# Performance work log

Measured on AMD Instinct MI355X. Metric: run time of the kernel, lower is better.

Reference implementation:

```python
import jax, jax.numpy as jnp
import numpy as np

B = 128
H = 512
S_TOK = 512
S_DESC = 128
N_NODES = 65536
MARGIN = 0.05
COS_EPS = 1e-8


def setup_inputs() -> dict:
    key = jax.random.key(0)
    ks = jax.random.split(key, 26)
    sc = 1.0 / np.sqrt(H)
    inp = {
        "token_feat": jax.random.normal(ks[0], (B, S_TOK, H), jnp.float32),
        "token_len": jnp.maximum(jax.random.randint(ks[1], (B,), 0, S_TOK), 1),
        "node_h": jax.random.normal(ks[2], (N_NODES, H), jnp.float32),
        "seg_ids": jnp.sort(jax.random.randint(ks[3], (N_NODES,), 0, B)),
        "desc_anchor_feat": jax.random.normal(ks[4], (B, S_DESC, H), jnp.float32),
        "desc_anchor_len": jnp.maximum(jax.random.randint(ks[5], (B,), 0, S_DESC), 1),
        "desc_neg_feat": jax.random.normal(ks[6], (B, S_DESC, H), jnp.float32),
        "desc_neg_len": jnp.maximum(jax.random.randint(ks[7], (B,), 0, S_DESC), 1),
        # attention params: Linear(H,H) weight/bias, Linear(H,1) weight/bias
        "Wt": jax.random.normal(ks[8], (H, H), jnp.float32) * sc,
        "bt": jax.random.normal(ks[9], (H,), jnp.float32) * sc,
        "vt": jax.random.normal(ks[10], (H,), jnp.float32) * sc,
        "ct": jax.random.normal(ks[11], (), jnp.float32) * sc,
        "Wa": jax.random.normal(ks[12], (H, H), jnp.float32) * sc,
        "ba": jax.random.normal(ks[13], (H,), jnp.float32) * sc,
        "va": jax.random.normal(ks[14], (H,), jnp.float32) * sc,
        "ca": jax.random.normal(ks[15], (), jnp.float32) * sc,
        "Wd": jax.random.normal(ks[16], (H, H), jnp.float32) * sc,
        "bd": jax.random.normal(ks[17], (H,), jnp.float32) * sc,
        "vd": jax.random.normal(ks[18], (H,), jnp.float32) * sc,
        "cd": jax.random.normal(ks[19], (), jnp.float32) * sc,
        "Wf": jax.random.normal(ks[20], (2 * H, H), jnp.float32) * sc,
        "bf": jax.random.normal(ks[21], (H,), jnp.float32) * sc,
    }
    return inp


def masked_attn_pool(feat, lens, W, b, v, c):
    # feat: [B,S,H]; lens: [B]. Masked softmax attention pooling == the
    # per-sample masked_select + softmax + bmm loop, vectorized.
    logits = jnp.einsum("bsh,h->bs", jnp.tanh(jnp.einsum("bsh,hk->bsk", feat, W) + b), v) + c
    mask = jnp.arange(feat.shape[1])[None, :] < lens[:, None]
    logits = jnp.where(mask, logits, -jnp.inf)
    w = jax.nn.softmax(logits, axis=1)  # [B,S]
    return jnp.einsum("bs,bsh->bh", w, feat)


def segment_attn_pool(h, seg, W, b, v, c, num_segments):
    # h: [N,H] packed node states; seg: [N] sample id. Per-segment softmax attn
    # pooling == the per-sample slice + softmax + bmm loop over tree_node_num.
    logits = jnp.tanh(h @ W + b) @ v + c  # [N]
    m = jax.ops.segment_max(logits, seg, num_segments=num_segments)
    e = jnp.exp(logits - m[seg])
    denom = jax.ops.segment_sum(e, seg, num_segments=num_segments)
    w = e / denom[seg]
    return jax.ops.segment_sum(w[:, None] * h, seg, num_segments=num_segments)


def cosine_sim(a, b):
    na = jnp.maximum(jnp.linalg.norm(a, axis=1), COS_EPS)
    nb = jnp.maximum(jnp.linalg.norm(b, axis=1), COS_EPS)
    return jnp.sum(a * b, axis=1) / (na * nb)


def reference(token_feat, token_len, node_h, seg_ids, desc_anchor_feat,
              desc_anchor_len, desc_neg_feat, desc_neg_len,
              Wt, bt, vt, ct, Wa, ba, va, ca, Wd, bd, vd, cd, Wf, bf):
    # token modality (use_token_attn, then use_tanh)
    tok = jnp.tanh(masked_attn_pool(token_feat, token_len, Wt, bt, vt, ct))
    # AST modality: use_tanh applies to node states BEFORE attention
    hn = jnp.tanh(node_h)
    ast = jnp.tanh(segment_attn_pool(hn, seg_ids, Wa, ba, va, ca, B))
    code_feat = jnp.tanh(jnp.concatenate([tok, ast], axis=1) @ Wf + bf)
    # desc modality: attn pool, use_tanh, then the extra unconditional tanh
    da = jnp.tanh(jnp.tanh(masked_attn_pool(desc_anchor_feat, desc_anchor_len, Wd, bd, vd, cd)))
    dn = jnp.tanh(jnp.tanh(masked_attn_pool(desc_neg_feat, desc_neg_len, Wd, bd, vd, cd)))
    anchor_sim = cosine_sim(code_feat, da)
    neg_sim = cosine_sim(code_feat, dn)
    loss = jnp.mean(jnp.maximum(MARGIN - anchor_sim + neg_sim, 1e-6))
    return loss
```

## Files before the change

kernel.cpp:

```cpp
#include <hip/hip_runtime.h>
#include <math.h>

#define HDIM 512
#define BATCH 128

typedef _Float16 f16x8 __attribute__((ext_vector_type(8)));
typedef float f32x4 __attribute__((ext_vector_type(4)));

__device__ __forceinline__ float fast_tanh(float x) {
  float e = __expf(2.0f * x);
  return 1.0f - 2.0f / (e + 1.0f);
}

__device__ __forceinline__ void gload_lds16(const void* g, void* l) {
  __builtin_amdgcn_global_load_lds(
      (const __attribute__((address_space(1))) unsigned int*)g,
      (__attribute__((address_space(3))) unsigned int*)l, 16, 0, 0);
}

__global__ __launch_bounds__(256) void cvt_w3_kernel(
    const float* __restrict__ Wt, const float* __restrict__ Wa,
    const float* __restrict__ Wd, _Float16* __restrict__ W2t,
    _Float16* __restrict__ W2a, _Float16* __restrict__ W2d) {
  const int i = blockIdx.x * 256 + threadIdx.x;
  if (i >= 512 * 64) return;
  const float* W = (blockIdx.y == 0) ? Wt : (blockIdx.y == 1) ? Wa : Wd;
  _Float16* W2 = (blockIdx.y == 0) ? W2t : (blockIdx.y == 1) ? W2a : W2d;
  const int n = i & 511, g = i >> 9;
  const int kt = g >> 2, kc = g & 3;
  f16x8 h;
#pragma unroll
  for (int j = 0; j < 8; ++j)
    h[j] = (_Float16)W[(size_t)(kt * 32 + kc * 8 + j) * HDIM + n];
  char* dst = (char*)W2 + (size_t)kt * 32768 + n * 64 + ((kc * 16) ^ ((n & 3) << 4));
  *(f16x8*)dst = h;
}

__global__ __launch_bounds__(512, 1) void gemm_logits_merged_kernel(
    const float* __restrict__ A_tok, const float* __restrict__ A_node,
    const float* __restrict__ A_da, const float* __restrict__ A_dn,
    const _Float16* __restrict__ W2t, const _Float16* __restrict__ W2a,
    const _Float16* __restrict__ W2d,
    const float* __restrict__ bt, const float* __restrict__ vt,
    const float* __restrict__ ba, const float* __restrict__ va,
    const float* __restrict__ bd, const float* __restrict__ vd,
    float* __restrict__ logits_tok, float* __restrict__ logits_node,
    float* __restrict__ logits_desc) {
  __shared__ __align__(16) _Float16 As[2][128 * 32];
  __shared__ __align__(16) _Float16 Bs[2][512 * 32];

  const int tid = threadIdx.x;
  const int raw = (int)blockIdx.x;
  const int swz = (raw & 7) * 160 + (raw >> 3);

  int id, mb;
  if (swz < 512)       { id = 0; mb = swz; }
  else if (swz < 1024) { id = 1; mb = swz - 512; }
  else if (swz < 1152) { id = 2; mb = swz - 1024; }
  else                 { id = 3; mb = swz - 1152; }
  const float* A = (id == 0) ? A_tok : (id == 1) ? A_node : (id == 2) ? A_da : A_dn;
  const _Float16* W2 = (id == 0) ? W2t : (id == 1) ? W2a : W2d;
  const float* bias = (id == 0) ? bt : (id == 1) ? ba : bd;
  const float* vvec = (id == 0) ? vt : (id == 1) ? va : vd;
  float* logits = (id == 0) ? logits_tok
                : (id == 1) ? logits_node
                : (id == 2) ? logits_desc : (logits_desc + 16384);
  const bool do_tanh = (id == 1);
  const size_t m0 = (size_t)mb * 128;

  const int lane = tid & 63, wid = tid >> 6;
  const int tx = lane & 15, qd = lane >> 4;

  const int arow = tid >> 2;
  const int apart = tid & 3;
  const float* arowp = A + (m0 + arow) * HDIM + apart * 8;
  const int awbyte = arow * 64 + ((apart * 16) ^ ((arow & 3) << 4));

  f32x4 acc[8][4];
#pragma unroll
  for (int i = 0; i < 8; ++i)
#pragma unroll
    for (int j = 0; j < 4; ++j) acc[i][j] = (f32x4){0.f, 0.f, 0.f, 0.f};

  float4 ar0, ar1;
  auto LOAD_A = [&](int t) {
    const float* p = arowp + t * 32;
    ar0 = ((const float4*)p)[0];
    ar1 = ((const float4*)p)[1];
  };
  auto STAGE_B = [&](int buf, int t) {
    const char* b = (const char*)W2 + (size_t)t * 32768;
#pragma unroll
    for (int p = 0; p < 4; ++p)
      gload_lds16(b + tid * 16 + p * 8192, (char*)Bs[buf] + tid * 16 + p * 8192);
  };
  auto WRITE_A = [&](int buf) {
    float v0 = ar0.x, v1 = ar0.y, v2 = ar0.z, v3 = ar0.w;
    float v4 = ar1.x, v5 = ar1.y, v6 = ar1.z, v7 = ar1.w;
    if (do_tanh) {
      v0 = fast_tanh(v0); v1 = fast_tanh(v1); v2 = fast_tanh(v2); v3 = fast_tanh(v3);
      v4 = fast_tanh(v4); v5 = fast_tanh(v5); v6 = fast_tanh(v6); v7 = fast_tanh(v7);
    }
    f16x8 h;
    h[0] = (_Float16)v0; h[1] = (_Float16)v1; h[2] = (_Float16)v2; h[3] = (_Float16)v3;
    h[4] = (_Float16)v4; h[5] = (_Float16)v5; h[6] = (_Float16)v6; h[7] = (_Float16)v7;
    *(f16x8*)((char*)As[buf] + awbyte) = h;
  };
  auto COMPUTE = [&](int buf) {
    f16x8 aF[8], bF[4];
#pragma unroll
    for (int i = 0; i < 8; ++i) {
      const int row = i * 16 + tx;
      aF[i] = *(const f16x8*)((const char*)As[buf] + row * 64 + ((qd * 16) ^ ((row & 3) << 4)));
    }
#pragma unroll
    for (int j = 0; j < 4; ++j) {
      const int n = wid * 64 + j * 16 + tx;
      bF[j] = *(const f16x8*)((const char*)Bs[buf] + n * 64 + ((qd * 16) ^ ((n & 3) << 4)));
    }
    __builtin_amdgcn_s_setprio(1);
#pragma unroll
    for (int i = 0; i < 8; ++i)
#pragma unroll
      for (int j = 0; j < 4; ++j)
        acc[i][j] = __builtin_amdgcn_mfma_f32_16x16x32_f16(aF[i], bF[j], acc[i][j], 0, 0, 0);
    __builtin_amdgcn_s_setprio(0);
  };

  LOAD_A(0);
  STAGE_B(0, 0);
  WRITE_A(0);
  __syncthreads();

  for (int t = 0; t < 16; ++t) {
    const int cur = t & 1;
    if (t < 15) {
      LOAD_A(t + 1);
      STAGE_B(cur ^ 1, t + 1);
    }
    COMPUTE(cur);
    if (t < 15) WRITE_A(cur ^ 1);
    __syncthreads();
  }

  float vv[4], bb[4];
#pragma unroll
  for (int j = 0; j < 4; ++j) {
    const int n = wid * 64 + j * 16 + tx;
    vv[j] = vvec[n];
    bb[j] = bias[n];
  }
  float* red = (float*)As;
#pragma unroll
  for (int i = 0; i < 8; ++i) {
#pragma unroll
    for (int r = 0; r < 4; ++r) {
      float s = 0.0f;
#pragma unroll
      for (int j = 0; j < 4; ++j)
        s = fmaf(vv[j], fast_tanh(acc[i][j][r] + bb[j]), s);
      s += __shfl_xor(s, 1);
      s += __shfl_xor(s, 2);
      s += __shfl_xor(s, 4);
      s += __shfl_xor(s, 8);
      if (tx == 0) red[wid * 128 + i * 16 + qd * 4 + r] = s;
    }
  }
  __syncthreads();
  if (tid < 128) {
    float tot = 0.0f;
#pragma unroll
    for (int w = 0; w < 8; ++w) tot += red[w * 128 + tid];
    logits[m0 + tid] = tot;
  }
}


__global__ void zero_kernel(float* __restrict__ p, int n) {
  const int i = blockIdx.x * 256 + threadIdx.x;
  if (i < n) p[i] = 0.0f;
}

__global__ void seg_bounds_kernel(const int* __restrict__ seg, int N,
                                  int* __restrict__ seg_start) {
  const int b = threadIdx.x;
  if (b > BATCH) return;
  int lo = 0, hi = N;
  while (lo < hi) {
    const int mid = (lo + hi) >> 1;
    if (seg[mid] < b) lo = mid + 1; else hi = mid;
  }
  seg_start[b] = lo;
}

__global__ __launch_bounds__(256) void softmax_all_kernel(
    float* __restrict__ ltok, float* __restrict__ ldesc,
    float* __restrict__ lnode, const int* __restrict__ tlen,
    const int* __restrict__ dalen, const int* __restrict__ dnlen,
    const int* __restrict__ seg_start) {
  __shared__ float smax[4], ssum[4];
  const int b = blockIdx.x, mode = blockIdx.y, tid = threadIdx.x;
  float* l;
  int s0, s1, fill_end;
  if (mode == 0)      { l = ltok + (size_t)b * 512;          s0 = 0; s1 = tlen[b];  fill_end = 512; }
  else if (mode == 1) { l = ldesc + (size_t)b * 128;         s0 = 0; s1 = dalen[b]; fill_end = 128; }
  else if (mode == 2) { l = ldesc + 16384 + (size_t)b * 128; s0 = 0; s1 = dnlen[b]; fill_end = 128; }
  else                { l = lnode; s0 = seg_start[b]; s1 = seg_start[b + 1]; fill_end = -1; }

  float mymax = -1e30f;
  for (int s = s0 + tid; s < s1; s += 256) mymax = fmaxf(mymax, l[s]);
#pragma unroll
  for (int off = 32; off; off >>= 1) mymax = fmaxf(mymax, __shfl_xor(mymax, off));
  if ((tid & 63) == 0) smax[tid >> 6] = mymax;
  __syncthreads();
  const float bmax = fmaxf(fmaxf(smax[0], smax[1]), fmaxf(smax[2], smax[3]));
  float mysum = 0.0f;
  for (int s = s0 + tid; s < s1; s += 256) mysum += __expf(l[s] - bmax);
#pragma unroll
  for (int off = 32; off; off >>= 1) mysum += __shfl_xor(mysum, off);
  if ((tid & 63) == 0) ssum[tid >> 6] = mysum;
  __syncthreads();
  const float inv = 1.0f / (ssum[0] + ssum[1] + ssum[2] + ssum[3]);
  for (int s = s0 + tid; s < s1; s += 256) l[s] = __expf(l[s] - bmax) * inv;
  if (fill_end > 0)
    for (int s = s1 + tid; s < fill_end; s += 256) l[s] = 0.0f;
}

__global__ __launch_bounds__(256) void pool_masked_all_kernel(
    const float* __restrict__ tok_feat, const float* __restrict__ da_feat,
    const float* __restrict__ dn_feat, const float* __restrict__ ltok,
    const float* __restrict__ ldesc, float* __restrict__ tok_pool,
    float* __restrict__ da_pool, float* __restrict__ dn_pool) {
  const int b = blockIdx.x, c = blockIdx.y, tid = threadIdx.x;
  const float* feat;
  const float* w;
  float* out;
  int S, s0;
  if (c < 8)       { feat = tok_feat; S = 512; w = ltok + (size_t)b * 512;          out = tok_pool; s0 = c * 64; }
  else if (c < 10) { feat = da_feat;  S = 128; w = ldesc + (size_t)b * 128;         out = da_pool;  s0 = (c - 8) * 64; }
  else             { feat = dn_feat;  S = 128; w = ldesc + 16384 + (size_t)b * 128; out = dn_pool;  s0 = (c - 10) * 64; }
  const int h = tid * 2;
  const float* fb = feat + (size_t)b * S * HDIM + h;
  float ax = 0.0f, ay = 0.0f;
  for (int s = s0; s < s0 + 64; ++s) {
    const float wsc = w[s];
    if (wsc != 0.0f) {
      const float2 f = *(const float2*)(fb + (size_t)s * HDIM);
      ax = fmaf(wsc, f.x, ax);
      ay = fmaf(wsc, f.y, ay);
    }
  }
  atomicAdd(&out[b * HDIM + h], ax);
  atomicAdd(&out[b * HDIM + h + 1], ay);
}

__global__ __launch_bounds__(256) void pool_seg_kernel(
    const float* __restrict__ node_h, const float* __restrict__ w,
    const int* __restrict__ seg_start, float* __restrict__ pool) {
  const int b = blockIdx.x, c = blockIdx.y, tid = threadIdx.x;
  const int h = tid * 2;
  const int s0 = seg_start[b], s1 = seg_start[b + 1];
  const int nseg = s1 - s0;
  const int chunk = (nseg + (int)gridDim.y - 1) / (int)gridDim.y;
  const int a0 = s0 + c * chunk;
  const int a1 = min(s1, a0 + chunk);
  float ax = 0.0f, ay = 0.0f;
  for (int s = a0; s < a1; ++s) {
    const float wsc = w[s];
    const float2 f = *(const float2*)(node_h + (size_t)s * HDIM + h);
    ax = fmaf(wsc, fast_tanh(f.x), ax);
    ay = fmaf(wsc, fast_tanh(f.y), ay);
  }
  atomicAdd(&pool[b * HDIM + h], ax);
  atomicAdd(&pool[b * HDIM + h + 1], ay);
}

__global__ __launch_bounds__(256) void code_gemm_kernel(
    const float* __restrict__ tok_pool, const float* __restrict__ ast_pool,
    const float* __restrict__ Wf, float* __restrict__ parts) {
  __shared__ float catS[128][65];
  __shared__ float4 wfS[64][32];
  const int nb = blockIdx.x, kb = blockIdx.y, tid = threadIdx.x;
  const int k0 = kb * 64;
  const float* src = (k0 < 512) ? (tok_pool + k0) : (ast_pool + (k0 - 512));
  for (int i = tid; i < 128 * 16; i += 256) {
    const int r = i >> 4, c4 = i & 15;
    const float4 v = *(const float4*)(src + (size_t)r * HDIM + c4 * 4);
    catS[r][c4 * 4 + 0] = fast_tanh(v.x);
    catS[r][c4 * 4 + 1] = fast_tanh(v.y);
    catS[r][c4 * 4 + 2] = fast_tanh(v.z);
    catS[r][c4 * 4 + 3] = fast_tanh(v.w);
  }
  for (int i = tid; i < 64 * 32; i += 256) {
    const int r = i >> 5, c = i & 31;
    wfS[r][c] = *(const float4*)(Wf + (size_t)(k0 + r) * HDIM + nb * 128 + c * 4);
  }
  __syncthreads();
  const int tb = tid >> 4, tn = tid & 15;
  const int b0 = tb * 8, n0l = tn * 8;
  float acc[8][8];
#pragma unroll
  for (int i = 0; i < 8; ++i)
#pragma unroll
    for (int j = 0; j < 8; ++j) acc[i][j] = 0.0f;
  for (int k = 0; k < 64; ++k) {
    float a[8];
#pragma unroll
    for (int i = 0; i < 8; ++i) a[i] = catS[b0 + i][k];
    const float4 w0 = wfS[k][tn * 2], w1 = wfS[k][tn * 2 + 1];
    const float wv[8] = {w0.x, w0.y, w0.z, w0.w, w1.x, w1.y, w1.z, w1.w};
#pragma unroll
    for (int i = 0; i < 8; ++i)
#pragma unroll
      for (int j = 0; j < 8; ++j) acc[i][j] = fmaf(a[i], wv[j], acc[i][j]);
  }
  float* dst = parts + ((size_t)kb * 128) * HDIM + nb * 128;
#pragma unroll
  for (int i = 0; i < 8; ++i) {
    const float4 o0 = {acc[i][0], acc[i][1], acc[i][2], acc[i][3]};
    const float4 o1 = {acc[i][4], acc[i][5], acc[i][6], acc[i][7]};
    *(float4*)(dst + (size_t)(b0 + i) * HDIM + n0l) = o0;
    *(float4*)(dst + (size_t)(b0 + i) * HDIM + n0l + 4) = o1;
  }
}

__global__ __launch_bounds__(256) void sims_kernel(
    const float* __restrict__ parts, const float* __restrict__ bfv,
    const float* __restrict__ da_pool, const float* __restrict__ dn_pool,
    float* __restrict__ terms) {
  __shared__ float sr[4][5];
  const int b = blockIdx.x, tid = threadIdx.x;
  float c2 = 0, a2 = 0, n2 = 0, ca = 0, cn = 0;
  for (int i = tid; i < HDIM; i += 256) {
    float pre = bfv[i];
#pragma unroll
    for (int kb = 0; kb < 16; ++kb)
      pre += parts[((size_t)kb * 128 + b) * HDIM + i];
    const float cf = fast_tanh(pre);
    const float av = fast_tanh(fast_tanh(da_pool[(size_t)b * HDIM + i]));
    const float nv = fast_tanh(fast_tanh(dn_pool[(size_t)b * HDIM + i]));
    c2 = fmaf(cf, cf, c2); a2 = fmaf(av, av, a2); n2 = fmaf(nv, nv, n2);
    ca = fmaf(cf, av, ca); cn = fmaf(cf, nv, cn);
  }
#pragma unroll
  for (int off = 32; off; off >>= 1) {
    c2 += __shfl_xor(c2, off); a2 += __shfl_xor(a2, off); n2 += __shfl_xor(n2, off);
    ca += __shfl_xor(ca, off); cn += __shfl_xor(cn, off);
  }
  const int wv = tid >> 6;
  if ((tid & 63) == 0) {
    sr[wv][0] = c2; sr[wv][1] = a2; sr[wv][2] = n2; sr[wv][3] = ca; sr[wv][4] = cn;
  }
  __syncthreads();
  if (tid == 0) {
    c2 = sr[0][0] + sr[1][0] + sr[2][0] + sr[3][0];
    a2 = sr[0][1] + sr[1][1] + sr[2][1] + sr[3][1];
    n2 = sr[0][2] + sr[1][2] + sr[2][2] + sr[3][2];
    ca = sr[0][3] + sr[1][3] + sr[2][3] + sr[3][3];
    cn = sr[0][4] + sr[1][4] + sr[2][4] + sr[3][4];
    const float nc = fmaxf(sqrtf(c2), 1e-8f);
    const float na = fmaxf(sqrtf(a2), 1e-8f);
    const float nn = fmaxf(sqrtf(n2), 1e-8f);
    terms[b] = fmaxf(0.05f - ca / (nc * na) + cn / (nc * nn), 1e-6f);
  }
}

__global__ void loss_kernel(const float* __restrict__ terms, float* __restrict__ out) {
  const int tid = threadIdx.x;
  float v = terms[tid];
#pragma unroll
  for (int off = 32; off; off >>= 1) v += __shfl_xor(v, off);
  __shared__ float sr[2];
  if ((tid & 63) == 0) sr[tid >> 6] = v;
  __syncthreads();
  if (tid == 0) out[0] = (sr[0] + sr[1]) * (1.0f / (float)BATCH);
}


extern "C" void kernel_launch(void* const* d_in, const int* in_sizes, int n_in,
                              void* d_out, int out_size, void* d_ws, size_t ws_size,
                              hipStream_t stream) {
  (void)in_sizes; (void)n_in; (void)out_size; (void)ws_size;
  const float* token_feat = (const float*)d_in[0];
  const int*   token_len  = (const int*)d_in[1];
  const float* node_h     = (const float*)d_in[2];
  const int*   seg_ids    = (const int*)d_in[3];
  const float* da_feat    = (const float*)d_in[4];
  const int*   da_len     = (const int*)d_in[5];
  const float* dn_feat    = (const float*)d_in[6];
  const int*   dn_len     = (const int*)d_in[7];
  const float* Wt = (const float*)d_in[8];
  const float* bt = (const float*)d_in[9];
  const float* vt = (const float*)d_in[10];
  const float* Wa = (const float*)d_in[12];
  const float* ba = (const float*)d_in[13];
  const float* va = (const float*)d_in[14];
  const float* Wd = (const float*)d_in[16];
  const float* bd = (const float*)d_in[17];
  const float* vd = (const float*)d_in[18];
  const float* Wf  = (const float*)d_in[20];
  const float* bfv = (const float*)d_in[21];

  const int MTOK = 65536;
  const int MDESC2 = 32768;
  const int NNODES = 65536;

  float* ws = (float*)d_ws;
  float* logits_tok  = ws;
  float* logits_node = logits_tok + MTOK;
  float* logits_desc = logits_node + NNODES;
  float* tok_pool    = logits_desc + MDESC2;
  float* ast_pool    = tok_pool + 128 * HDIM;
  float* da_pool     = ast_pool + 128 * HDIM;
  float* dn_pool     = da_pool + 128 * HDIM;
  float* terms       = dn_pool + 128 * HDIM;
  int*   seg_start   = (int*)(terms + 128);
  float* parts       = (float*)(seg_start + 256);
  _Float16* W2t = (_Float16*)(parts + 16 * 128 * HDIM);
  _Float16* W2a = W2t + HDIM * HDIM;
  _Float16* W2d = W2a + HDIM * HDIM;

  zero_kernel<<<dim3((4 * 128 * HDIM + 255) / 256), 256, 0, stream>>>(tok_pool, 4 * 128 * HDIM);
  seg_bounds_kernel<<<1, 256, 0, stream>>>(seg_ids, NNODES, seg_start);
  cvt_w3_kernel<<<dim3(128, 3), 256, 0, stream>>>(Wt, Wa, Wd, W2t, W2a, W2d);

  gemm_logits_merged_kernel<<<1280, 512, 0, stream>>>(
      token_feat, node_h, da_feat, dn_feat, W2t, W2a, W2d,
      bt, vt, ba, va, bd, vd, logits_tok, logits_node, logits_desc);

  softmax_all_kernel<<<dim3(BATCH, 4), 256, 0, stream>>>(
      logits_tok, logits_desc, logits_node, token_len, da_len, dn_len, seg_start);

  pool_masked_all_kernel<<<dim3(BATCH, 12), 256, 0, stream>>>(
      token_feat, da_feat, dn_feat, logits_tok, logits_desc,
      tok_pool, da_pool, dn_pool);
  pool_seg_kernel<<<dim3(BATCH, 4), 256, 0, stream>>>(
      node_h, logits_node, seg_start, ast_pool);

  code_gemm_kernel<<<dim3(4, 16), 256, 0, stream>>>(tok_pool, ast_pool, Wf, parts);
  sims_kernel<<<BATCH, 256, 0, stream>>>(parts, bfv, da_pool, dn_pool, terms);
  loss_kernel<<<1, 128, 0, stream>>>(terms, (float*)d_out);
}
```

Before: 353.9 us.

## Retile logits GEMM to 256x256 blocks with K=64 steps and atomic reduction

The fused logits GEMM moves from 128-row by full-512-column tiles with K=32 to 256x256 tiles with K=64. The weight layout is changed to match, using 128-byte rows and an 8-way XOR swizzle. The two column halves now combine their partial logits with atomicAdd into a workspace that is zeroed first, which replaces the shared-memory cross-wave reduction. The main loop uses manual vmcnt waits and raw barriers instead of __syncthreads, to overlap loads with MFMA work and halve the number of iterations. The trade-offs are atomics, extra A re-reads across the two column blocks, larger LDS use, and a bigger zero-fill.

```diff
diff --git a/kernel.cpp b/kernel.cpp
--- a/kernel.cpp
+++ b/kernel.cpp
@@ -27,16 +27,16 @@
   const float* W = (blockIdx.y == 0) ? Wt : (blockIdx.y == 1) ? Wa : Wd;
   _Float16* W2 = (blockIdx.y == 0) ? W2t : (blockIdx.y == 1) ? W2a : W2d;
   const int n = i & 511, g = i >> 9;
-  const int kt = g >> 2, kc = g & 3;
+  const int kt = g >> 3, cc = g & 7;
   f16x8 h;
 #pragma unroll
   for (int j = 0; j < 8; ++j)
-    h[j] = (_Float16)W[(size_t)(kt * 32 + kc * 8 + j) * HDIM + n];
-  char* dst = (char*)W2 + (size_t)kt * 32768 + n * 64 + ((kc * 16) ^ ((n & 3) << 4));
+    h[j] = (_Float16)W[(size_t)(kt * 64 + cc * 8 + j) * HDIM + n];
+  char* dst = (char*)W2 + ((size_t)kt * 512 + n) * 128 + ((cc * 16) ^ ((n & 7) << 4));
   *(f16x8*)dst = h;
 }
 
-__global__ __launch_bounds__(512, 1) void gemm_logits_merged_kernel(
+__global__ __launch_bounds__(512, 1) void gemm_logits_merged2_kernel(
     const float* __restrict__ A_tok, const float* __restrict__ A_node,
     const float* __restrict__ A_da, const float* __restrict__ A_dn,
     const _Float16* __restrict__ W2t, const _Float16* __restrict__ W2a,
@@ -46,18 +46,19 @@
     const float* __restrict__ bd, const float* __restrict__ vd,
     float* __restrict__ logits_tok, float* __restrict__ logits_node,
     float* __restrict__ logits_desc) {
-  __shared__ __align__(16) _Float16 As[2][128 * 32];
-  __shared__ __align__(16) _Float16 Bs[2][512 * 32];
+  __shared__ __align__(16) _Float16 As[2][256 * 64];
+  __shared__ __align__(16) _Float16 Bs[2][256 * 64];
 
   const int tid = threadIdx.x;
   const int raw = (int)blockIdx.x;
   const int swz = (raw & 7) * 160 + (raw >> 3);
 
-  int id, mb;
-  if (swz < 512)       { id = 0; mb = swz; }
-  else if (swz < 1024) { id = 1; mb = swz - 512; }
-  else if (swz < 1152) { id = 2; mb = swz - 1024; }
-  else                 { id = 3; mb = swz - 1152; }
+  int id, local;
+  if (swz < 512)       { id = 0; local = swz; }
+  else if (swz < 1024) { id = 1; local = swz - 512; }
+  else if (swz < 1152) { id = 2; local = swz - 1024; }
+  else                 { id = 3; local = swz - 1152; }
+  const int mb = local >> 1, nb = local & 1;
   const float* A = (id == 0) ? A_tok : (id == 1) ? A_node : (id == 2) ? A_da : A_dn;
   const _Float16* W2 = (id == 0) ? W2t : (id == 1) ? W2a : W2d;
   const float* bias = (id == 0) ? bt : (id == 1) ? ba : bd;
@@ -66,15 +67,22 @@
                 : (id == 1) ? logits_node
                 : (id == 2) ? logits_desc : (logits_desc + 16384);
   const bool do_tanh = (id == 1);
-  const size_t m0 = (size_t)mb * 128;
+  const size_t m0 = (size_t)mb * 256;
+  const int n0 = nb * 256;
 
   const int lane = tid & 63, wid = tid >> 6;
   const int tx = lane & 15, qd = lane >> 4;
-
-  const int arow = tid >> 2;
-  const int apart = tid & 3;
-  const float* arowp = A + (m0 + arow) * HDIM + apart * 8;
-  const int awbyte = arow * 64 + ((apart * 16) ^ ((arow & 3) << 4));
+  const int wm = wid >> 2;
+  const int wn = wid & 3;
+
+  const int arow = tid >> 1, ahalf = tid & 1;
+  const float* aptr = A + (m0 + arow) * HDIM + ahalf * 32;
+  int awb[4];
+#pragma unroll
+  for (int q = 0; q < 4; ++q)
+    awb[q] = arow * 128 + ((ahalf * 64 + q * 16) ^ ((arow & 7) << 4));
+
+  const char* gB = (const char*)W2 + (size_t)n0 * 128;
 
   f32x4 acc[8][4];
 #pragma unroll
@@ -82,75 +90,101 @@
 #pragma unroll
     for (int j = 0; j < 4; ++j) acc[i][j] = (f32x4){0.f, 0.f, 0.f, 0.f};
 
-  float4 ar0, ar1;
+  float4 ar0, ar1, ar2, ar3, ar4, ar5, ar6, ar7;
   auto LOAD_A = [&](int t) {
-    const float* p = arowp + t * 32;
-    ar0 = ((const float4*)p)[0];
-    ar1 = ((const float4*)p)[1];
+    const float4* p = (const float4*)(aptr + t * 64);
+    ar0 = p[0]; ar1 = p[1]; ar2 = p[2]; ar3 = p[3];
+    ar4 = p[4]; ar5 = p[5]; ar6 = p[6]; ar7 = p[7];
   };
   auto STAGE_B = [&](int buf, int t) {
-    const char* b = (const char*)W2 + (size_t)t * 32768;
+    const char* b = gB + (size_t)t * 65536;
 #pragma unroll
     for (int p = 0; p < 4; ++p)
       gload_lds16(b + tid * 16 + p * 8192, (char*)Bs[buf] + tid * 16 + p * 8192);
   };
   auto WRITE_A = [&](int buf) {
-    float v0 = ar0.x, v1 = ar0.y, v2 = ar0.z, v3 = ar0.w;
-    float v4 = ar1.x, v5 = ar1.y, v6 = ar1.z, v7 = ar1.w;
-    if (do_tanh) {
-      v0 = fast_tanh(v0); v1 = fast_tanh(v1); v2 = fast_tanh(v2); v3 = fast_tanh(v3);
-      v4 = fast_tanh(v4); v5 = fast_tanh(v5); v6 = fast_tanh(v6); v7 = fast_tanh(v7);
-    }
-    f16x8 h;
-    h[0] = (_Float16)v0; h[1] = (_Float16)v1; h[2] = (_Float16)v2; h[3] = (_Float16)v3;
-    h[4] = (_Float16)v4; h[5] = (_Float16)v5; h[6] = (_Float16)v6; h[7] = (_Float16)v7;
-    *(f16x8*)((char*)As[buf] + awbyte) = h;
+    float v[8];
+    float4 t0 = ar0, t1 = ar1, t2 = ar2, t3 = ar3;
+#pragma unroll
+    for (int pair = 0; pair < 4; ++pair) {
+      const float4 x = (pair == 0) ? ar0 : (pair == 1) ? ar2 : (pair == 2) ? ar4 : ar6;
+      const float4 y = (pair == 0) ? ar1 : (pair == 1) ? ar3 : (pair == 2) ? ar5 : ar7;
+      v[0] = x.x; v[1] = x.y; v[2] = x.z; v[3] = x.w;
+      v[4] = y.x; v[5] = y.y; v[6] = y.z; v[7] = y.w;
+      f16x8 h;
+      if (do_tanh) {
+#pragma unroll
+        for (int j = 0; j < 8; ++j) h[j] = (_Float16)fast_tanh(v[j]);
+      } else {
+#pragma unroll
+        for (int j = 0; j < 8; ++j) h[j] = (_Float16)v[j];
+      }
+      *(f16x8*)((char*)As[buf] + awb[pair]) = h;
+    }
+    (void)t0; (void)t1; (void)t2; (void)t3;
   };
   auto COMPUTE = [&](int buf) {
     f16x8 aF[8], bF[4];
 #pragma unroll
-    for (int i = 0; i < 8; ++i) {
-      const int row = i * 16 + tx;
-      aF[i] = *(const f16x8*)((const char*)As[buf] + row * 64 + ((qd * 16) ^ ((row & 3) << 4)));
-    }
-#pragma unroll
-    for (int j = 0; j < 4; ++j) {
-      const int n = wid * 64 + j * 16 + tx;
-      bF[j] = *(const f16x8*)((const char*)Bs[buf] + n * 64 + ((qd * 16) ^ ((n & 3) << 4)));
-    }
-    __builtin_amdgcn_s_setprio(1);
-#pragma unroll
-    for (int i = 0; i < 8; ++i)
-#pragma unroll
-      for (int j = 0; j < 4; ++j)
-        acc[i][j] = __builtin_amdgcn_mfma_f32_16x16x32_f16(aF[i], bF[j], acc[i][j], 0, 0, 0);
-    __builtin_amdgcn_s_setprio(0);
+    for (int ks = 0; ks < 2; ++ks) {
+#pragma unroll
+      for (int i = 0; i < 8; ++i) {
+        const int row = wm * 128 + i * 16 + tx;
+        aF[i] = *(const f16x8*)((const char*)As[buf] + row * 128 +
+                                ((ks * 64 + qd * 16) ^ ((row & 7) << 4)));
+      }
+#pragma unroll
+      for (int j = 0; j < 4; ++j) {
+        const int n = wn * 64 + j * 16 + tx;
+        bF[j] = *(const f16x8*)((const char*)Bs[buf] + n * 128 +
+                                ((ks * 64 + qd * 16) ^ ((n & 7) << 4)));
+      }
+      __builtin_amdgcn_s_setprio(1);
+#pragma unroll
+      for (int i = 0; i < 8; ++i)
+#pragma unroll
+        for (int j = 0; j < 4; ++j)
+          acc[i][j] = __builtin_amdgcn_mfma_f32_16x16x32_f16(aF[i], bF[j], acc[i][j], 0, 0, 0);
+      __builtin_amdgcn_s_setprio(0);
+    }
   };
 
   LOAD_A(0);
   STAGE_B(0, 0);
+  asm volatile("s_waitcnt vmcnt(4)" ::: "memory");
   WRITE_A(0);
-  __syncthreads();
-
-  for (int t = 0; t < 16; ++t) {
+
+#pragma unroll
+  for (int t = 0; t < 8; ++t) {
     const int cur = t & 1;
-    if (t < 15) {
+    if (t < 7) {
       LOAD_A(t + 1);
       STAGE_B(cur ^ 1, t + 1);
-    }
+      asm volatile("s_waitcnt vmcnt(12)" ::: "memory");
+    } else {
+      asm volatile("s_waitcnt vmcnt(0)" ::: "memory");
+    }
+    asm volatile("s_waitcnt lgkmcnt(0)" ::: "memory");
+    asm volatile("" ::: "memory");
+    __builtin_amdgcn_s_barrier();
+    asm volatile("" ::: "memory");
     COMPUTE(cur);
-    if (t < 15) WRITE_A(cur ^ 1);
-    __syncthreads();
+    if (t < 7) {
+      asm volatile("s_waitcnt vmcnt(4)" ::: "memory");
+      WRITE_A(cur ^ 1);
+    }
+    asm volatile("" ::: "memory");
+    __builtin_amdgcn_s_barrier();
+    asm volatile("" ::: "memory");
   }
 
   float vv[4], bb[4];
 #pragma unroll
   for (int j = 0; j < 4; ++j) {
-    const int n = wid * 64 + j * 16 + tx;
+    const int n = n0 + wn * 64 + j * 16 + tx;
     vv[j] = vvec[n];
     bb[j] = bias[n];
   }
-  float* red = (float*)As;
 #pragma unroll
   for (int i = 0; i < 8; ++i) {
 #pragma unroll
@@ -163,15 +197,9 @@
       s += __shfl_xor(s, 2);
       s += __shfl_xor(s, 4);
       s += __shfl_xor(s, 8);
-      if (tx == 0) red[wid * 128 + i * 16 + qd * 4 + r] = s;
-    }
-  }
-  __syncthreads();
-  if (tid < 128) {
-    float tot = 0.0f;
-#pragma unroll
-    for (int w = 0; w < 8; ++w) tot += red[w * 128 + tid];
-    logits[m0 + tid] = tot;
+      if (tx == 0)
+        atomicAdd(&logits[m0 + wm * 128 + i * 16 + qd * 4 + r], s);
+    }
   }
 }
 
@@ -420,11 +448,12 @@
   _Float16* W2a = W2t + HDIM * HDIM;
   _Float16* W2d = W2a + HDIM * HDIM;
 
-  zero_kernel<<<dim3((4 * 128 * HDIM + 255) / 256), 256, 0, stream>>>(tok_pool, 4 * 128 * HDIM);
+  const int ZTOT = MTOK + NNODES + MDESC2 + 4 * 128 * HDIM;
+  zero_kernel<<<dim3((ZTOT + 255) / 256), 256, 0, stream>>>(ws, ZTOT);
   seg_bounds_kernel<<<1, 256, 0, stream>>>(seg_ids, NNODES, seg_start);
   cvt_w3_kernel<<<dim3(128, 3), 256, 0, stream>>>(Wt, Wa, Wd, W2t, W2a, W2d);
 
-  gemm_logits_merged_kernel<<<1280, 512, 0, stream>>>(
+  gemm_logits_merged2_kernel<<<1280, 512, 0, stream>>>(
       token_feat, node_h, da_feat, dn_feat, W2t, W2a, W2d,
       bt, vt, ba, va, bd, vd, logits_tok, logits_node, logits_desc);
 
```

Result: slower. 412.2 us (+16.5%).
